# Optimization experiments

Hardware: AMD Instinct MI355X
Metric: run time of the kernel (lower is better)

## Reference

```python
import jax, jax.numpy as jnp
import numpy as np

DEPTH = 13                 # tree depth -> N = 2**DEPTH - 1 reaches (heap layout, outlet = node 0)
N = 2 ** DEPTH - 1         # 8191 reaches
T = 2048                   # timesteps


def setup_inputs() -> dict:
    key = jax.random.key(0)
    ks = jax.random.split(key, 8)
    u = lambda k, shape, lo, hi: jax.random.uniform(k, shape, minval=lo, maxval=hi, dtype=jnp.float32)
    return {
        "lateral_inflows": u(ks[0], (T, N), 0.0, 2.0),     # m^3/s lateral inflow per reach
        "manning_n":       u(ks[1], (N,), 0.025, 0.06),    # Manning roughness
        "lengths":         u(ks[2], (N,), 1000.0, 5000.0), # reach length [m]
        "slopes":          u(ks[3], (N,), 1e-4, 1e-2),     # bed slope (>= 1e-4 as in source)
        "width_coefs":     u(ks[4], (N,), 3.0, 10.0),      # w = wc * Q**we  (power-law geometry)
        "width_exps":      u(ks[5], (N,), 0.4, 0.6),
        "depth_coefs":     u(ks[6], (N,), 0.2, 0.5),       # h = dc * Q**de
        "depth_exps":      u(ks[7], (N,), 0.3, 0.45),
        "dt": 3600,                                        # routing timestep [s]
    }


def _mc_outflow(I_new, I_old, O_old, n, L, S, wc, we, dc, de, dt):
    """Variable-parameter Muskingum-Cunge update for one vector of reaches."""
    Qr = jnp.maximum(0.5 * (I_new + O_old), 1e-3)          # reference discharge
    h = dc * Qr ** de                                       # hydraulic depth
    w = wc * Qr ** we                                       # top width
    v = h ** (2.0 / 3.0) * jnp.sqrt(S) / n                  # Manning velocity
    c = jnp.maximum((5.0 / 3.0) * v, 1e-3)                  # kinematic celerity
    K = L / c                                               # travel time
    X = jnp.clip(0.5 * (1.0 - Qr / (w * S * c * L)), 0.0, 0.5)
    den = 2.0 * K * (1.0 - X) + dt
    C1 = (dt - 2.0 * K * X) / den
    C2 = (dt + 2.0 * K * X) / den
    C3 = (2.0 * K * (1.0 - X) - dt) / den
    return jnp.maximum(C1 * I_new + C2 * I_old + C3 * O_old, 0.0)


def reference(lateral_inflows, manning_n, lengths, slopes, width_coefs, width_exps,
              depth_coefs, depth_exps, dt):
    dtf = jnp.float32(dt)
    Np = lateral_inflows.shape[1]
    params = (manning_n, lengths, slopes, width_coefs, width_exps, depth_coefs, depth_exps)

    def step(carry, lat_t):
        I_old, O_old = carry                                # [N] prev inflow / outflow
        Q = jnp.zeros(Np, dtype=lat_t.dtype)                # new outflows this timestep
        I_all = jnp.zeros(Np, dtype=lat_t.dtype)
        # process levels leaves -> root (reverse topological order over the DAG)
        for l in range(DEPTH - 1, -1, -1):
            s, e = 2 ** l - 1, 2 ** (l + 1) - 1             # nodes of level l
            if l == DEPTH - 1:
                up = jnp.float32(0.0)                        # headwater reaches
            else:
                cs, ce = 2 ** (l + 1) - 1, 2 ** (l + 2) - 1  # children = level l+1
                up = Q[cs:ce:2] + Q[cs + 1:ce:2]             # sum of 2 upstream discharges
            I_new = lat_t[s:e] + up
            O_new = _mc_outflow(I_new, I_old[s:e], O_old[s:e],
                                *(p[s:e] for p in params), dtf)
            Q = Q.at[s:e].set(O_new)
            I_all = I_all.at[s:e].set(I_new)
        return (I_all, Q), Q[0]                              # outlet = root (index 0)

    init = (jnp.zeros(Np, jnp.float32), jnp.zeros(Np, jnp.float32))
    _, outlet_Q = jax.lax.scan(step, init, lateral_inflows)
    return outlet_Q                                          # [T]
```

## Files before the change

### kernel.cpp

```cpp
#include <hip/hip_runtime.h>


#define NN 8191
#define TT 2048
#define FBATCH 32
#define NBLK 39
#define BTHREADS 256

#define FLAGS_FOFF 16773120ull
#define REQ_BYTES  67106816ull
#define FLAG_STRIDE 16

#if __has_builtin(__builtin_amdgcn_exp2f)
__device__ __forceinline__ float fexp2(float x) { return __builtin_amdgcn_exp2f(x); }
#else
__device__ __forceinline__ float fexp2(float x) { return exp2f(x); }
#endif
#if __has_builtin(__builtin_amdgcn_logf)
__device__ __forceinline__ float flog2(float x) { return __builtin_amdgcn_logf(x); }
#else
__device__ __forceinline__ float flog2(float x) { return log2f(x); }
#endif
#if __has_builtin(__builtin_amdgcn_rcpf)
__device__ __forceinline__ float frcp(float x) { return __builtin_amdgcn_rcpf(x); }
#else
__device__ __forceinline__ float frcp(float x) { return 1.0f / x; }
#endif

__constant__ int g_level[NBLK] = {
    12,12,12,12,12,12,12,12,12,12,12,12,12,12,12,12,
    11,11,11,11,11,11,11,11,
    10,10,10,10,
    9,9,
    8,7,6,5,4,3,2,1,0};
__constant__ int g_cnt[NBLK] = {
    256,256,256,256,256,256,256,256,256,256,256,256,256,256,256,256,
    256,256,256,256,256,256,256,256,
    256,256,256,256,
    256,256,
    256,128,64,32,16,8,4,2,1};
__constant__ int g_first[13] = {38,37,36,35,34,33,32,31,30,28,24,16,0};
__constant__ unsigned long long g_off[13] = {
    16773120ull, 16769024ull, 16760832ull, 16744448ull, 16711680ull,
    16646144ull, 16515072ull, 16252928ull, 15728640ull, 14680064ull,
    12582912ull, 8388608ull, 0ull};

__device__ __forceinline__ void waitflags(const unsigned int* fa, const unsigned int* fb,
                                          unsigned int target)
{
    while (true) {
        unsigned int a = __hip_atomic_load(fa, __ATOMIC_RELAXED, __HIP_MEMORY_SCOPE_AGENT);
        unsigned int b = fb ? __hip_atomic_load(fb, __ATOMIC_RELAXED, __HIP_MEMORY_SCOPE_AGENT)
                            : a;
        if (a >= target && b >= target) break;
        __builtin_amdgcn_s_sleep(1);
    }
    __builtin_amdgcn_sched_barrier(0);
    asm volatile("" ::: "memory");
}

__global__ void zero_flags(unsigned int* flags)
{
    for (int i = threadIdx.x; i < NBLK * 4 * FLAG_STRIDE; i += 256) flags[i] = 0;
}

__global__ __launch_bounds__(BTHREADS, 1)
void pipe_kernel(const float* __restrict__ lat,
                 const float* __restrict__ nman,
                 const float* __restrict__ len,
                 const float* __restrict__ slp,
                 const float* __restrict__ wcf,
                 const float* __restrict__ wex,
                 const float* __restrict__ dcf,
                 const float* __restrict__ dex,
                 const int*   __restrict__ dtp,
                 float*       __restrict__ out,
                 float*       __restrict__ ws)
{
    const int bid = blockIdx.x;
    const int tid = threadIdx.x;
    const int lvl = g_level[bid];
    const int cnt = g_cnt[bid];
    const int W   = tid >> 6;
    const int wn  = cnt - W * 64;
    if (wn <= 0) return;

    const bool active = (tid < cnt);
    const int B = bid - g_first[lvl];
    const int m = B * 256 + (active ? tid : 0);
    const int node = ((1 << lvl) - 1) + m;
    const int wbase = B * 256 + W * 64;

    unsigned int* flags = (unsigned int*)(ws + FLAGS_FOFF);
    unsigned int* myflag = flags + ((size_t)bid * 4 + W) * FLAG_STRIDE;

    const bool haschild = (lvl < 12);
    const unsigned int* fa = nullptr;
    const unsigned int* fb = nullptr;
    if (haschild) {
        const int Fp = g_first[lvl + 1];
        const int nw = wn < 64 ? wn : 64;
        const int p0 = (2 * wbase) >> 6;
        const int p1 = (2 * wbase + 2 * nw - 1) >> 6;
        fa = flags + ((size_t)(Fp + (p0 >> 2)) * 4 + (p0 & 3)) * FLAG_STRIDE;
        fb = (p1 != p0)
           ? flags + ((size_t)(Fp + (p1 >> 2)) * 4 + (p1 & 3)) * FLAG_STRIDE
           : nullptr;
    }

    const int myW = 1 << lvl;
    const int childW = 1 << (lvl + 1);
    float* myBuf = ws + g_off[lvl];
    const unsigned long long* childBuf =
        haschild ? (const unsigned long long*)(ws + g_off[lvl + 1]) : nullptr;

    const float dtf = (float)dtp[0];

    float em, eme, tkc, p1c, p2c;
    float Iold = 0.0f, Oold = 0.0f;
    {
        float n = nman[node], L = len[node], S = slp[node];
        float wc = wcf[node], we = wex[node], dc = dcf[node], de = dex[node];
        float dc23 = fexp2(0.6666667f * flog2(dc));
        float cc = 1.6666667f * dc23 * sqrtf(S) * frcp(n);
        float e23 = 0.6666667f * de;
        em  = -e23;
        eme = 1.0f - we - 2.0f * e23;
        tkc = 2.0f * L * frcp(cc);
        float k1 = 0.5f * frcp(S * L * wc * cc);
        p1c = 0.5f * tkc;
        p2c = k1 * tkc;
    }

    float laA[FBATCH], laB[FBATCH];
    unsigned long long cvA[FBATCH], cvB[FBATCH];
    unsigned int fva = 0xFFFFFFFFu, fvb = 0xFFFFFFFFu;

#define LATBURST(dst, tb)                                                      \
    if (active) {                                                              \
        _Pragma("unroll")                                                      \
        for (int k = 0; k < FBATCH; ++k) {                                     \
            const float* lp_ = lat + (size_t)((tb) + k) * NN + node;           \
            asm volatile("global_load_dword %0, %1, off"                       \
                         : "=v"(dst[k]) : "v"(lp_));                           \
        }                                                                      \
    }

#define CHILDBURST(dst, tb)                                                    \
    if (haschild && active) {                                                  \
        _Pragma("unroll")                                                      \
        for (int k = 0; k < FBATCH; ++k) {                                     \
            const unsigned long long* cp_ =                                    \
                childBuf + (((size_t)((tb) + k) * childW) >> 1) + m;           \
            asm volatile("global_load_dwordx2 %0, %1, off sc0 sc1"             \
                         : "=v"(dst[k]) : "v"(cp_));                           \
        }                                                                      \
    }

#define FLAGLOAD()                                                             \
    if (haschild) {                                                            \
        asm volatile("global_load_dword %0, %1, off sc0 sc1"                   \
                     : "=v"(fva) : "v"(fa));                                   \
        if (fb)                                                                \
            asm volatile("global_load_dword %0, %1, off sc0 sc1"               \
                         : "=v"(fvb) : "v"(fb));                               \
    }

#define FLAGCHECK(TGT)                                                         \
    if (haschild) {                                                            \
        asm volatile("s_waitcnt vmcnt(0)"                                      \
                     : "+v"(fva), "+v"(fvb) :: "memory");                      \
        unsigned int tgt_ = (unsigned int)(TGT);                               \
        if (fva < tgt_ || fvb < tgt_) waitflags(fa, fb, tgt_);                 \
    }

#define UPDS(laC, cvC, T0, K0, K1)                                             \
    if (active) {                                                              \
        _Pragma("unroll")                                                      \
        for (int k = (K0); k < (K1); ++k) {                                    \
            float ch_ = 0.0f;                                                  \
            if (haschild) {                                                    \
                float c0_ = __uint_as_float((unsigned int)(cvC[k] & 0xffffffffull)); \
                float c1_ = __uint_as_float((unsigned int)(cvC[k] >> 32));     \
                ch_ = c0_ + c1_;                                               \
            }                                                                  \
            float Inew = laC[k] + ch_;                                         \
            float Qr = fmaxf(0.5f * (Inew + Oold), 1e-3f);                     \
            float lg = flog2(Qr);                                              \
            float E1  = fexp2(em * lg);                                        \
            float E12 = fexp2(eme * lg);                                       \
            float twoK = tkc * E1;                                             \
            float A = fmaxf(p1c * E1 - p2c * E12, 0.0f);                       \
            float den = (twoK + dtf) - A;                                      \
            float r = frcp(den);                                               \
            float s1 = Inew + Iold - Oold;                                     \
            float s2 = s1 - 2.0f * Inew;                                       \
            float pre = twoK * Oold + dtf * s1;                                \
            float num = pre + A * s2;                                          \
            float O = fmaxf(num * r, 0.0f);                                    \
            Iold = Inew; Oold = O;                                             \
            if (lvl > 0)                                                       \
                __hip_atomic_store(myBuf + (size_t)((T0) + k) * myW + m, O,    \
                                   __ATOMIC_RELAXED, __HIP_MEMORY_SCOPE_AGENT);\
            else                                                               \
                out[(T0) + k] = O;                                             \
        }                                                                      \
    }

#define PHASE(laC, cvC, laN, cvN, T0)                                          \
    do {                                                                       \
        const int t1_ = (T0) + FBATCH;                                         \
        const bool hn_ = (t1_ < TT);                                           \
        fva = 0xFFFFFFFFu; fvb = 0xFFFFFFFFu;                                  \
        UPDS(laC, cvC, (T0), 0, 10);                                           \
        if (hn_) { LATBURST(laN, t1_); FLAGLOAD(); }                           \
        UPDS(laC, cvC, (T0), 10, 20);                                          \
        if (hn_) {                                                             \
            FLAGCHECK(t1_ + FBATCH);                                           \
            __builtin_amdgcn_sched_barrier(0);                                 \
            CHILDBURST(cvN, t1_);                                              \
            __builtin_amdgcn_sched_barrier(0);                                 \
        }                                                                      \
        UPDS(laC, cvC, (T0), 20, FBATCH);                                      \
        asm volatile("s_waitcnt vmcnt(0)" ::: "memory");                       \
        __builtin_amdgcn_sched_barrier(0);                                     \
        if (lvl > 0 && (tid & 63) == 0)                                        \
            __hip_atomic_store(myflag, (unsigned int)((T0) + FBATCH),          \
                               __ATOMIC_RELAXED, __HIP_MEMORY_SCOPE_AGENT);    \
    } while (0)

    LATBURST(laA, 0);
    if (haschild) waitflags(fa, fb, (unsigned int)FBATCH);
    CHILDBURST(cvA, 0);
    asm volatile("s_waitcnt vmcnt(0)" ::: "memory");
    __builtin_amdgcn_sched_barrier(0);

    for (int t0 = 0; t0 < TT; t0 += 2 * FBATCH) {
        PHASE(laA, cvA, laB, cvB, t0);
        PHASE(laB, cvB, laA, cvA, t0 + FBATCH);
    }
#undef LATBURST
#undef CHILDBURST
#undef FLAGLOAD
#undef FLAGCHECK
#undef UPDS
#undef PHASE
}

#define NTHREADS 1024
__device__ __forceinline__ float mc_update_fb(float Inew, float Iold, float Oold,
                                              float em, float tkc, float ex, float k1,
                                              float dtf)
{
    float Qr = fmaxf(0.5f * (Inew + Oold), 1e-3f);
    float lg = flog2(Qr);
    float twoK = tkc * fexp2(em * lg);
    float X = fmaxf(0.5f - k1 * fexp2(ex * lg), 0.0f);
    float A = twoK * X;
    float B = twoK - A;
    float r = frcp(B + dtf);
    float C1 = (dtf - A) * r;
    float C2 = (dtf + A) * r;
    float C3 = (B - dtf) * r;
    return fmaxf(C1 * Inew + C2 * Iold + C3 * Oold, 0.0f);
}

__global__ __launch_bounds__(NTHREADS)
void route_kernel(const float* __restrict__ lat,
                  const float* __restrict__ nman,
                  const float* __restrict__ len,
                  const float* __restrict__ slp,
                  const float* __restrict__ wcf,
                  const float* __restrict__ wex,
                  const float* __restrict__ dcf,
                  const float* __restrict__ dex,
                  const int*   __restrict__ dtp,
                  float*       __restrict__ out)
{
    __shared__ float Osh[NN];
    const int tid = threadIdx.x;
    const float dtf = (float)dtp[0];

    int nodes[8];
    nodes[0] = 4095 + tid;
    nodes[1] = 5119 + tid;
    nodes[2] = 6143 + tid;
    nodes[3] = 7167 + tid;
    nodes[4] = 2047 + tid;
    nodes[5] = 3071 + tid;
    nodes[6] = 1023 + tid;
    nodes[7] = (tid < 1023) ? tid : 0;

    float em[8], tkc[8], ex[8], k1[8];
    float Ireg[8], Oreg[8];
#pragma unroll
    for (int k = 0; k < 8; ++k) {
        int i = nodes[k];
        float n = nman[i], L = len[i], S = slp[i];
        float wc = wcf[i], we = wex[i], dc = dcf[i], de = dex[i];
        float dc23 = fexp2(0.6666667f * flog2(dc));
        float cc = 1.6666667f * dc23 * sqrtf(S) * frcp(n);
        float e23 = 0.6666667f * de;
        em[k]  = -e23;
        tkc[k] = 2.0f * L * frcp(cc);
        ex[k]  = 1.0f - we - e23;
        k1[k]  = 0.5f * frcp(S * L * wc * cc);
        Ireg[k] = 0.0f; Oreg[k] = 0.0f;
    }
    for (int i = tid; i < NN; i += NTHREADS) Osh[i] = 0.0f;
    __syncthreads();

    for (int t = 0; t < TT; ++t) {
        const float* __restrict__ latt = lat + (size_t)t * NN;
#pragma unroll
        for (int k = 0; k < 4; ++k) {
            int i = nodes[k];
            float Inew = latt[i];
            float O = mc_update_fb(Inew, Ireg[k], Oreg[k], em[k], tkc[k], ex[k], k1[k], dtf);
            Ireg[k] = Inew; Oreg[k] = O; Osh[i] = O;
        }
        __syncthreads();
#pragma unroll
        for (int k = 4; k < 6; ++k) {
            int i = nodes[k];
            float Inew = latt[i] + Osh[2 * i + 1] + Osh[2 * i + 2];
            float O = mc_update_fb(Inew, Ireg[k], Oreg[k], em[k], tkc[k], ex[k], k1[k], dtf);
            Ireg[k] = Inew; Oreg[k] = O; Osh[i] = O;
        }
        __syncthreads();
        {
            int i = nodes[6];
            float Inew = latt[i] + Osh[2 * i + 1] + Osh[2 * i + 2];
            float O = mc_update_fb(Inew, Ireg[6], Oreg[6], em[6], tkc[6], ex[6], k1[6], dtf);
            Ireg[6] = Inew; Oreg[6] = O; Osh[i] = O;
        }
        __syncthreads();
        for (int l = 9; l >= 0; --l) {
            int s = (1 << l) - 1;
            int e = (1 << (l + 1)) - 1;
            if (tid >= s && tid < e) {
                int i = tid;
                float Inew = latt[i] + Osh[2 * i + 1] + Osh[2 * i + 2];
                float O = mc_update_fb(Inew, Ireg[7], Oreg[7], em[7], tkc[7], ex[7], k1[7], dtf);
                Ireg[7] = Inew; Oreg[7] = O; Osh[i] = O;
            }
            __syncthreads();
        }
        if (tid == 0) out[t] = Oreg[7];
    }
}

extern "C" void kernel_launch(void* const* d_in, const int* in_sizes, int n_in,
                              void* d_out, int out_size, void* d_ws, size_t ws_size,
                              hipStream_t stream) {
    const float* lat  = (const float*)d_in[0];
    const float* nman = (const float*)d_in[1];
    const float* len  = (const float*)d_in[2];
    const float* slp  = (const float*)d_in[3];
    const float* wcf  = (const float*)d_in[4];
    const float* wex  = (const float*)d_in[5];
    const float* dcf  = (const float*)d_in[6];
    const float* dex  = (const float*)d_in[7];
    const int*   dtp  = (const int*)d_in[8];
    float* out = (float*)d_out;

    if (ws_size >= REQ_BYTES) {
        float* ws = (float*)d_ws;
        unsigned int* flags = (unsigned int*)(ws + FLAGS_FOFF);
        zero_flags<<<dim3(1), dim3(256), 0, stream>>>(flags);
        pipe_kernel<<<dim3(NBLK), dim3(BTHREADS), 0, stream>>>(
            lat, nman, len, slp, wcf, wex, dcf, dex, dtp, out, ws);
    } else {
        route_kernel<<<dim3(1), dim3(NTHREADS), 0, stream>>>(
            lat, nman, len, slp, wcf, wex, dcf, dex, dtp, out);
    }
}
```

Baseline: 442.5 us.

## Predict next-step powers off the critical path and correct with Taylor polynomial

Moves the transcendental log/exp and reciprocal work out of the serial time-recurrence dependency chain. Each step uses a predicted next outflow, computed from the previous coefficients, to precompute the powers and reciprocal one step ahead. The actual step then applies a cubic Taylor correction in the relative deviation, plus two Newton iterations for the reciprocal. This shortens the per-step latency chain but adds extra ALU work. It is also an approximation whose accuracy depends on the prediction error, clamped to ±0.5.

```diff
diff --git a/kernel.cpp b/kernel.cpp
--- a/kernel.cpp
+++ b/kernel.cpp
@@ -116,7 +116,7 @@
 
     const float dtf = (float)dtp[0];
 
-    float em, eme, tkc, p1c, p2c;
+    float em, eme, tkc, p1c, p2c, c2e, c3e, c2m, c3m;
     float Iold = 0.0f, Oold = 0.0f;
     {
         float n = nman[node], L = len[node], S = slp[node];
@@ -130,11 +130,22 @@
         float k1 = 0.5f * frcp(S * L * wc * cc);
         p1c = 0.5f * tkc;
         p2c = k1 * tkc;
-    }
+        c2e = 0.5f * em * (em - 1.0f);
+        c3e = c2e * (em - 2.0f) * 0.33333333f;
+        c2m = 0.5f * eme * (eme - 1.0f);
+        c3m = c2m * (eme - 2.0f) * 0.33333333f;
+    }
+
+    float Rh = 0.0f, E1h = 0.0f, E12h = 0.0f, rh = 0.0f;
+    float tks = 0.0f, As = 0.0f, rs = 0.0f;
 
     float laA[FBATCH], laB[FBATCH];
     unsigned long long cvA[FBATCH], cvB[FBATCH];
     unsigned int fva = 0xFFFFFFFFu, fvb = 0xFFFFFFFFu;
+
+#define CHSUM(cvw)                                                             \
+    (__uint_as_float((unsigned int)((cvw) & 0xffffffffull)) +                  \
+     __uint_as_float((unsigned int)((cvw) >> 32)))
 
 #define LATBURST(dst, tb)                                                      \
     if (active) {                                                              \
@@ -174,36 +185,61 @@
         if (fva < tgt_ || fvb < tgt_) waitflags(fa, fb, tgt_);                 \
     }
 
+#define PACKCALC(QH)                                                           \
+    {                                                                          \
+        float lgh_ = flog2(QH);                                                \
+        E1h = fexp2(em * lgh_);                                                \
+        E12h = fexp2(eme * lgh_);                                              \
+        Rh = frcp(QH);                                                         \
+        float tkh_ = tkc * E1h;                                                \
+        float Ah_ = fmaxf(fmaf(-p2c, E12h, p1c * E1h), 0.0f);                  \
+        float dnh_ = (tkh_ + dtf) - Ah_;                                       \
+        rh = frcp(dnh_);                                                       \
+    }
+
 #define UPDS(laC, cvC, T0, K0, K1)                                             \
     if (active) {                                                              \
         _Pragma("unroll")                                                      \
         for (int k = (K0); k < (K1); ++k) {                                    \
-            float ch_ = 0.0f;                                                  \
-            if (haschild) {                                                    \
-                float c0_ = __uint_as_float((unsigned int)(cvC[k] & 0xffffffffull)); \
-                float c1_ = __uint_as_float((unsigned int)(cvC[k] >> 32));     \
-                ch_ = c0_ + c1_;                                               \
-            }                                                                  \
+            float ch_ = haschild ? CHSUM(cvC[k]) : 0.0f;                       \
             float Inew = laC[k] + ch_;                                         \
             float Qr = fmaxf(0.5f * (Inew + Oold), 1e-3f);                     \
-            float lg = flog2(Qr);                                              \
-            float E1  = fexp2(em * lg);                                        \
-            float E12 = fexp2(eme * lg);                                       \
-            float twoK = tkc * E1;                                             \
-            float A = fmaxf(p1c * E1 - p2c * E12, 0.0f);                       \
-            float den = (twoK + dtf) - A;                                      \
-            float r = frcp(den);                                               \
-            float s1 = Inew + Iold - Oold;                                     \
-            float s2 = s1 - 2.0f * Inew;                                       \
-            float pre = twoK * Oold + dtf * s1;                                \
-            float num = pre + A * s2;                                          \
-            float O = fmaxf(num * r, 0.0f);                                    \
-            Iold = Inew; Oold = O;                                             \
+            float d_ = fmaf(Qr, Rh, -1.0f);                                    \
+            d_ = fminf(fmaxf(d_, -0.5f), 0.5f);                                \
+            float u1_ = fmaf(c3e, d_, c2e); u1_ = fmaf(u1_, d_, em);           \
+            float f1_ = fmaf(u1_, d_, 1.0f);                                   \
+            float u2_ = fmaf(c3m, d_, c2m); u2_ = fmaf(u2_, d_, eme);          \
+            float f2_ = fmaf(u2_, d_, 1.0f);                                   \
+            float E1_ = E1h * f1_;                                             \
+            float E12_ = E12h * f2_;                                           \
+            float twoK_ = tkc * E1_;                                           \
+            float A_ = fmaxf(fmaf(-p2c, E12_, p1c * E1_), 0.0f);               \
+            float den_ = (twoK_ + dtf) - A_;                                   \
+            float rn_ = fmaf(-den_, rh, 2.0f);                                 \
+            float r_ = rh * rn_;                                               \
+            rn_ = fmaf(-den_, r_, 2.0f);                                       \
+            r_ = r_ * rn_;                                                     \
+            float s1_ = (Inew + Iold) - Oold;                                  \
+            float s2_ = fmaf(-2.0f, Inew, s1_);                                \
+            float pre_ = fmaf(twoK_, Oold, dtf * s1_);                         \
+            float num_ = fmaf(A_, s2_, pre_);                                  \
+            float O_ = fmaxf(num_ * r_, 0.0f);                                 \
+              \
+            if (k + 1 < FBATCH) {                                              \
+                float po_ = fmaf(As, s2_, fmaf(tks, Oold, dtf * s1_));         \
+                float Op_ = fmaxf(po_ * rs, 0.0f);                             \
+                float chn_ = haschild ? CHSUM(cvC[k + 1]) : 0.0f;              \
+                float In1_ = laC[k + 1] + chn_;                                \
+                float Qh_ = fmaxf(0.5f * (In1_ + Op_), 1e-3f);                 \
+                PACKCALC(Qh_);                                                 \
+            }                                                                  \
+            tks = twoK_; As = A_; rs = r_;                                     \
+            Iold = Inew; Oold = O_;                                            \
             if (lvl > 0)                                                       \
-                __hip_atomic_store(myBuf + (size_t)((T0) + k) * myW + m, O,    \
+                __hip_atomic_store(myBuf + (size_t)((T0) + k) * myW + m, O_,   \
                                    __ATOMIC_RELAXED, __HIP_MEMORY_SCOPE_AGENT);\
             else                                                               \
-                out[(T0) + k] = O;                                             \
+                out[(T0) + k] = O_;                                            \
         }                                                                      \
     }
 
@@ -227,6 +263,13 @@
         if (lvl > 0 && (tid & 63) == 0)                                        \
             __hip_atomic_store(myflag, (unsigned int)((T0) + FBATCH),          \
                                __ATOMIC_RELAXED, __HIP_MEMORY_SCOPE_AGENT);    \
+           \
+        if (hn_ && active) {                                                   \
+            float chb_ = haschild ? CHSUM(cvN[0]) : 0.0f;                      \
+            float Ib_ = laN[0] + chb_;                                         \
+            float Qhb_ = fmaxf(0.5f * (Ib_ + Oold), 1e-3f);                    \
+            PACKCALC(Qhb_);                                                    \
+        }                                                                      \
     } while (0)
 
     LATBURST(laA, 0);
@@ -234,15 +277,26 @@
     CHILDBURST(cvA, 0);
     asm volatile("s_waitcnt vmcnt(0)" ::: "memory");
     __builtin_amdgcn_sched_barrier(0);
+    if (active) {
+        float ch0 = haschild ? CHSUM(cvA[0]) : 0.0f;
+        float I0 = laA[0] + ch0;
+        float Qh0 = fmaxf(0.5f * (I0 + Oold), 1e-3f);
+        PACKCALC(Qh0);
+        tks = tkc * E1h;
+        As = fmaxf(fmaf(-p2c, E12h, p1c * E1h), 0.0f);
+        rs = rh;
+    }
 
     for (int t0 = 0; t0 < TT; t0 += 2 * FBATCH) {
         PHASE(laA, cvA, laB, cvB, t0);
         PHASE(laB, cvB, laA, cvA, t0 + FBATCH);
     }
+#undef CHSUM
 #undef LATBURST
 #undef CHILDBURST
 #undef FLAGLOAD
 #undef FLAGCHECK
+#undef PACKCALC
 #undef UPDS
 #undef PHASE
 }
```

Result: slower. 551.0 us (+24.5%).
